# Kernel optimization log

Hardware: AMD Instinct MI355X
Metric: run time of the kernel (lower is better)

## Reference

```python
import jax, jax.numpy as jnp
import numpy as np

VOCAB_SIZE = 50000

def setup_inputs() -> dict:
    key = jax.random.key(0)
    # token index sequences: [batch, seq_len], values in [0, vocab)
    x = jax.random.randint(key, (2048, 200), 0, VOCAB_SIZE, dtype=jnp.int64)
    return {"x": x}

def reference(x) -> jnp.ndarray:
    # Faithful to: sum_{l} one_hot(x[b, l], V)  ->  [batch, vocab] count histogram.
    # Implemented as a scatter-add instead of materializing the
    # [batch, seq_len, vocab] one-hot tensor (same math, O(B*L) traffic on the
    # index side plus the [B, V] output).
    B, L = x.shape
    rows = jnp.broadcast_to(jnp.arange(B)[:, None], (B, L))  # [B, L]
    out = jnp.zeros((B, VOCAB_SIZE), dtype=jnp.float32)
    out = out.at[rows, x].add(jnp.float32(1.0))
    return out
```

## Files before the change

kernel.cpp:

```cpp
#include <hip/hip_runtime.h>

#define VOCAB 50000
#define SEQ   200
#define NF4   (VOCAB / 4)
#define NHW   (VOCAB / 16)

__global__ __launch_bounds__(256) void MultihotEmbedding_16458314678493_kernel(
    const int* __restrict__ x, float* __restrict__ out) {
  __shared__ unsigned hist[NHW];
  __shared__ int lidx[SEQ];
  __shared__ int ovf;

  const int row = blockIdx.x;
  const int t = threadIdx.x;
  float* __restrict__ orow = out + (size_t)row * VOCAB;

  for (int i = t; i < NHW; i += 256) hist[i] = 0u;
  if (t < SEQ / 4) ((int4*)lidx)[t] = ((const int4*)(x + row * SEQ))[t];
  if (t == 0) ovf = 0;
  __syncthreads();

  int myidx = -1, cnt = 0, first = 1;
  if (t < SEQ) myidx = lidx[t];
  for (int jj = 0; jj < SEQ / 4; ++jj) {
    const int4 q = ((const int4*)lidx)[jj];
    const int j0 = jj * 4;
    if (q.x == myidx) { cnt++; if (j0 + 0 < t) first = 0; }
    if (q.y == myidx) { cnt++; if (j0 + 1 < t) first = 0; }
    if (q.z == myidx) { cnt++; if (j0 + 2 < t) first = 0; }
    if (q.w == myidx) { cnt++; if (j0 + 3 < t) first = 0; }
  }
  if (t < SEQ && first) {
    atomicOr(&hist[myidx >> 4],
             (unsigned)(cnt < 3 ? cnt : 3) << ((myidx & 15) * 2));
    if (cnt > 3) atomicOr((unsigned*)&ovf, 1u);
  }
  __syncthreads();

  float4* __restrict__ o4 = (float4*)orow;
  for (int i = t; i < NF4; i += 256) {
    const unsigned b = (hist[i >> 2] >> ((i & 3) * 8)) & 0xFFu;
    float4 v;
    v.x = (float)(b & 3u);
    v.y = (float)((b >> 2) & 3u);
    v.z = (float)((b >> 4) & 3u);
    v.w = (float)((b >> 6) & 3u);
    o4[i] = v;
  }

  if (ovf) {
    __syncthreads();
    if (t < SEQ && first && cnt > 3) orow[myidx] = (float)cnt;
  }
}

extern "C" void kernel_launch(void* const* d_in, const int* in_sizes, int n_in,
                              void* d_out, int out_size, void* d_ws, size_t ws_size,
                              hipStream_t stream) {
  const int* x = (const int*)d_in[0];
  float* out = (float*)d_out;
  const int batch = in_sizes[0] / SEQ;
  MultihotEmbedding_16458314678493_kernel<<<batch, 256, 0, stream>>>(x, out);
}
```

Baseline: 412.2 us.

## Replace packed shared-memory histogram with per-thread register slot table

Replaces the 2-bit packed shared histogram over the full vocabulary with a small hashed slot table. Each vocab float4 group is owned by one thread, and up to four entries per owner are held in registers during the output write loop. Collisions beyond four spill to an overflow list that is scattered afterwards. This removes zeroing and reading a 12.5 KB shared array per block. In exchange, every output element now pays four compare/select operations.

```diff
diff --git a/kernel.cpp b/kernel.cpp
--- a/kernel.cpp
+++ b/kernel.cpp
@@ -3,21 +3,25 @@
 #define VOCAB 50000
 #define SEQ   200
 #define NF4   (VOCAB / 4)
-#define NHW   (VOCAB / 16)
+#define H     4
 
 __global__ __launch_bounds__(256) void MultihotEmbedding_16458314678493_kernel(
     const int* __restrict__ x, float* __restrict__ out) {
-  __shared__ unsigned hist[NHW];
   __shared__ int lidx[SEQ];
-  __shared__ int ovf;
+  __shared__ unsigned slots[H * 256];
+  __shared__ unsigned nslot[256];
+  __shared__ unsigned ovflist[SEQ];
+  __shared__ unsigned ovfn;
 
   const int row = blockIdx.x;
   const int t = threadIdx.x;
   float* __restrict__ orow = out + (size_t)row * VOCAB;
 
-  for (int i = t; i < NHW; i += 256) hist[i] = 0u;
   if (t < SEQ / 4) ((int4*)lidx)[t] = ((const int4*)(x + row * SEQ))[t];
-  if (t == 0) ovf = 0;
+#pragma unroll
+  for (int s = 0; s < H; ++s) slots[s * 256 + t] = 0xFF00u;
+  nslot[t] = 0u;
+  if (t == 0) ovfn = 0u;
   __syncthreads();
 
   int myidx = -1, cnt = 0, first = 1;
@@ -31,26 +35,49 @@
     if (q.w == myidx) { cnt++; if (j0 + 3 < t) first = 0; }
   }
   if (t < SEQ && first) {
-    atomicOr(&hist[myidx >> 4],
-             (unsigned)(cnt < 3 ? cnt : 3) << ((myidx & 15) * 2));
-    if (cnt > 3) atomicOr((unsigned*)&ovf, 1u);
+    const int owner = (myidx >> 2) & 255;
+    const unsigned key = (unsigned)(((myidx >> 10) << 2) | (myidx & 3));
+    const unsigned pos = atomicAdd(&nslot[owner], 1u);
+    if (pos < H) {
+      slots[pos * 256 + owner] = (key << 8) | (unsigned)cnt;
+    } else {
+      const unsigned o = atomicAdd(&ovfn, 1u);
+      ovflist[o] = ((unsigned)myidx << 8) | (unsigned)cnt;
+    }
   }
   __syncthreads();
 
+  const unsigned s0 = slots[0 * 256 + t];
+  const unsigned s1 = slots[1 * 256 + t];
+  const unsigned s2 = slots[2 * 256 + t];
+  const unsigned s3 = slots[3 * 256 + t];
+  const unsigned novf = ovfn;
+
   float4* __restrict__ o4 = (float4*)orow;
+#define APPLY(s)                                        \
+  do {                                                  \
+    const bool m = ((s) >> 10) == (unsigned)k;          \
+    const float c = (float)((s) & 255u);                \
+    const unsigned sub = ((s) >> 8) & 3u;               \
+    v.x = (m && sub == 0u) ? c : v.x;                   \
+    v.y = (m && sub == 1u) ? c : v.y;                   \
+    v.z = (m && sub == 2u) ? c : v.z;                   \
+    v.w = (m && sub == 3u) ? c : v.w;                   \
+  } while (0)
   for (int i = t; i < NF4; i += 256) {
-    const unsigned b = (hist[i >> 2] >> ((i & 3) * 8)) & 0xFFu;
-    float4 v;
-    v.x = (float)(b & 3u);
-    v.y = (float)((b >> 2) & 3u);
-    v.z = (float)((b >> 4) & 3u);
-    v.w = (float)((b >> 6) & 3u);
+    const int k = i >> 8;
+    float4 v = make_float4(0.f, 0.f, 0.f, 0.f);
+    APPLY(s0); APPLY(s1); APPLY(s2); APPLY(s3);
     o4[i] = v;
   }
+#undef APPLY
 
-  if (ovf) {
+  if (novf) {
     __syncthreads();
-    if (t < SEQ && first && cnt > 3) orow[myidx] = (float)cnt;
+    for (unsigned j = t; j < novf; j += 256) {
+      const unsigned e = ovflist[j];
+      orow[e >> 8] = (float)(e & 255u);
+    }
   }
 }
 
```

Measured after the change: 413.4 us. Within noise of the previous version (+0.3%).
